# Kernel optimization log

Measured on AMD Instinct MI355X. Metric: run time of the kernel, lower is better.

The kernel has to match this reference:

```python
import jax, jax.numpy as jnp
import numpy as np

B, N = 16, 4096
D_IN, D_OUT, HID, E = 128, 128, 256, 8
SG_HID = 16  # SharedGate hidden fixed at 16 in __init__


def setup_inputs() -> dict:
    key = jax.random.key(0)
    ks = jax.random.split(key, 6)
    s = 0.05
    return {
        "x": jax.random.normal(ks[0], (B, N, D_IN), dtype=jnp.float32),
        "active_experts": jnp.ones((B, E), dtype=jnp.int32),
        # SharedGate: fc1 [16, D_IN], fc2 [D_IN, 16] (torch Linear weight is [out, in])
        "sg_w1": jax.random.normal(ks[1], (SG_HID, D_IN), dtype=jnp.float32) * s,
        "sg_w2": jax.random.normal(ks[2], (D_IN, SG_HID), dtype=jnp.float32) * s,
        # TaskSpecificGate: E linears [1, D_IN] -> stacked [E, D_IN]
        "gate_w": jax.random.normal(ks[3], (E, D_IN), dtype=jnp.float32) * s,
        # Expert MLPs (no bias): fc1 [E, HID, D_IN], fc2 [E, D_OUT, HID]
        "exp_w1": jax.random.normal(ks[4], (E, HID, D_IN), dtype=jnp.float32) * s,
        "exp_w2": jax.random.normal(ks[5], (E, D_OUT, HID), dtype=jnp.float32) * s,
    }


def reference(x, active_experts, sg_w1, sg_w2, gate_w, exp_w1, exp_w2):
    b, n, d_in = x.shape
    xf = x.reshape(-1, d_in)  # [T, D_IN], T = B*N (node-level routing)

    # SharedGate with residual: fc2(relu(fc1(x))) + x
    shared = jnp.maximum(xf @ sg_w1.T, 0.0) @ sg_w2.T + xf  # [T, D_IN]

    # Task-specific gate: per-expert scalar scores, masked softmax over experts
    scores = (shared @ gate_w.T).reshape(b, n, -1)  # [B, N, E]
    mask = active_experts.astype(bool)[:, None, :]  # [B, 1, E]
    masked = jnp.where(mask, scores, -jnp.inf)
    weights = jax.nn.softmax(masked, axis=-1)  # [B, N, E]

    # All experts (dense): batched two-layer MLP per expert
    h = jnp.maximum(jnp.einsum("td,ehd->teh", xf, exp_w1), 0.0)  # [T, E, HID]
    out = jnp.einsum("teh,eoh->teo", h, exp_w2)  # [T, E, D_OUT]
    out_r = out.reshape(b, n, weights.shape[-1], -1)  # [B, N, E, D_OUT]

    # Gate-weighted combine over experts
    output_end = jnp.sum(out_r * weights[..., None], axis=2)  # [B, N, D_OUT]
    aux_loss = jnp.float32(0.0)  # sign=False
    return output_end, aux_loss
```

## Files before the change

kernel.cpp:

```cpp
#include <hip/hip_runtime.h>
#include <hip/hip_bf16.h>


typedef float f32x4 __attribute__((ext_vector_type(4)));
typedef short bf16x8 __attribute__((ext_vector_type(8)));

static __device__ __forceinline__ short f2bs(float f) {
  union { __hip_bfloat16 b; short s; } u;
  u.b = __float2bfloat16(f);
  return u.s;
}

static __device__ __forceinline__ unsigned pk2(float lo, float hi) {
  union { __hip_bfloat162 b; unsigned u; } t;
  t.b = __float22bfloat162_rn(make_float2(lo, hi));
  return t.u;
}


__global__ void prep_kernel(const float* __restrict__ sg_w1,
                            const float* __restrict__ sg_w2,
                            const float* __restrict__ gate_w,
                            const float* __restrict__ exp_w1,
                            const float* __restrict__ exp_w2,
                            short* __restrict__ ws_s) {
  int idx = blockIdx.x * 256 + threadIdx.x;
  if (idx < 262144) {
    int e = idx >> 15, rem = idx & 32767;
    int frag = rem >> 9, lane = (rem >> 3) & 63, j = rem & 7;
    int hid = (frag >> 2) * 16 + (lane & 15);
    int k   = (frag & 3) * 32 + (lane >> 4) * 8 + j;
    ws_s[idx] = f2bs(exp_w1[(e * 256 + hid) * 128 + k]);
  } else if (idx < 524288) {
    int i2 = idx - 262144;
    int e = i2 >> 15, rem = i2 & 32767;
    int frag = rem >> 9, lane = (rem >> 3) & 63, j = rem & 7;
    int lg = lane >> 4, l15 = lane & 15;
    int ks = frag >> 3;
    int oi = frag & 7;
    int o  = oi * 16 + l15;
    int h  = ks * 32 + (j < 4 ? lg * 4 + j : 16 + lg * 4 + (j - 4));
    ws_s[idx] = f2bs(exp_w2[(e * 128 + o) * 256 + h]);
  } else if (idx < 526336) {
    int i3 = idx - 524288;
    int k = i3 >> 9, lane = (i3 >> 3) & 63, j = i3 & 7;
    int lg = lane >> 4, l15 = lane & 15;
    ws_s[idx] = f2bs(sg_w1[l15 * 128 + k * 32 + lg * 8 + j]);
  } else if (idx < 528384) {
    int i4 = idx - 526336;
    int k = i4 >> 9, lane = (i4 >> 3) & 63, j = i4 & 7;
    int lg = lane >> 4, l15 = lane & 15;
    ws_s[idx] = (l15 < 8) ? f2bs(gate_w[l15 * 128 + k * 32 + lg * 8 + j]) : (short)0;
  } else if (idx < 528896) {
    int i5 = idx - 528384;
    int lane = (i5 >> 3) & 63, j = i5 & 7;
    int lg = lane >> 4, l15 = lane & 15;
    int kk = lg * 8 + j;
    if (l15 < 8 && kk < 16) {
      float acc = 0.f;
      for (int d = 0; d < 128; ++d) acc += gate_w[l15 * 128 + d] * sg_w2[d * 16 + kk];
      ws_s[idx] = f2bs(acc);
    } else {
      ws_s[idx] = 0;
    }
  }
}

__global__ __launch_bounds__(256, 2) void moe_kernel(
    const float* __restrict__ x, const int* __restrict__ active,
    const short* __restrict__ ws_s, float* __restrict__ out) {
  __shared__ __align__(16) short Abuf[2][4096];
  __shared__ short Ul[4][1280];

  const short* W1p  = ws_s;
  const short* W2p  = ws_s + 262144;
  const short* sg1p = ws_s + 524288;
  const short* gwp  = ws_s + 526336;
  const short* gcp  = ws_s + 528384;

  const int tid  = threadIdx.x;
  const int lane = tid & 63;
  const int wid  = tid >> 6;
  const int l15  = lane & 15;
  const int lg   = lane >> 4;
  const int tokw = blockIdx.x * 128 + wid * 32;

  auto stageA = [&](int buf, int c) {
#pragma unroll
    for (int t = 0; t < 2; ++t) {
      int i = wid * 2 + t;
      const short* s = W1p + ((size_t)c * 8 + i) * 512 + lane * 8;
      __builtin_amdgcn_global_load_lds(
          (const __attribute__((address_space(1))) void*)s,
          (__attribute__((address_space(3))) void*)(&Abuf[buf][i * 512]),
          16, 0, 0);
    }
  };
  auto loadB = [&](bf16x8 (&B)[8], int c) {
    const short* p = W2p + (size_t)c * 4096 + lane * 8;
#pragma unroll
    for (int oi = 0; oi < 8; ++oi)
      B[oi] = *(const bf16x8*)(p + oi * 512);
  };

  stageA(0, 0);

  short* Ulw = &Ul[wid][0];
  for (int i = lane; i < 640; i += 64) ((int*)Ulw)[i] = 0;

  bf16x8 xf[2][4];
  {
    int trow = tokw + l15;
#pragma unroll
    for (int m = 0; m < 2; ++m) {
      const float* xr = x + (size_t)(trow + m * 16) * 128;
#pragma unroll
      for (int k = 0; k < 4; ++k) {
        int c = k * 32 + lg * 8;
        float4 a = *(const float4*)(xr + c);
        float4 b = *(const float4*)(xr + c + 4);
        bf16x8 v;
        v[0] = f2bs(a.x); v[1] = f2bs(a.y); v[2] = f2bs(a.z); v[3] = f2bs(a.w);
        v[4] = f2bs(b.x); v[5] = f2bs(b.y); v[6] = f2bs(b.z); v[7] = f2bs(b.w);
        xf[m][k] = v;
      }
    }
  }
  __syncthreads();

  f32x4 wreg[2];
  {
    bf16x8 sgf[4], gwf[4];
#pragma unroll
    for (int k = 0; k < 4; ++k) {
      sgf[k] = *(const bf16x8*)(sg1p + k * 512 + lane * 8);
      gwf[k] = *(const bf16x8*)(gwp  + k * 512 + lane * 8);
    }
#pragma unroll
    for (int m = 0; m < 2; ++m) {
      f32x4 acc = {0.f, 0.f, 0.f, 0.f};
#pragma unroll
      for (int k = 0; k < 4; ++k)
        acc = __builtin_amdgcn_mfma_f32_16x16x32_bf16(xf[m][k], sgf[k], acc, 0, 0, 0);
#pragma unroll
      for (int r = 0; r < 4; ++r)
        Ulw[(m * 16 + lg * 4 + r) * 40 + l15] = f2bs(fmaxf(acc[r], 0.f));
    }
    f32x4 sc[2];
#pragma unroll
    for (int m = 0; m < 2; ++m) {
      f32x4 acc = {0.f, 0.f, 0.f, 0.f};
#pragma unroll
      for (int k = 0; k < 4; ++k)
        acc = __builtin_amdgcn_mfma_f32_16x16x32_bf16(xf[m][k], gwf[k], acc, 0, 0, 0);
      sc[m] = acc;
    }
    __syncthreads();
    bf16x8 gcf = *(const bf16x8*)(gcp + lane * 8);
#pragma unroll
    for (int m = 0; m < 2; ++m) {
      bf16x8 uf = *(const bf16x8*)(Ulw + (m * 16 + l15) * 40 + lg * 8);
      sc[m] = __builtin_amdgcn_mfma_f32_16x16x32_bf16(uf, gcf, sc[m], 0, 0, 0);
    }
    int b = tokw >> 12;
    float am = (l15 < 8 && active[b * 8 + l15] != 0) ? 0.f : -3.0e38f;
#pragma unroll
    for (int m = 0; m < 2; ++m) {
      f32x4 w4;
#pragma unroll
      for (int r = 0; r < 4; ++r) {
        float s = sc[m][r] + am;
        float mx = s;
        mx = fmaxf(mx, __shfl_xor(mx, 1));
        mx = fmaxf(mx, __shfl_xor(mx, 2));
        mx = fmaxf(mx, __shfl_xor(mx, 4));
        float p = __expf(s - mx);
        float su = p;
        su += __shfl_xor(su, 1);
        su += __shfl_xor(su, 2);
        su += __shfl_xor(su, 4);
        w4[r] = p / su;
      }
      wreg[m] = w4;
    }
  }

  f32x4 acc2[2][8];
#pragma unroll
  for (int m = 0; m < 2; ++m)
#pragma unroll
    for (int o = 0; o < 8; ++o)
      acc2[m][o] = {0.f, 0.f, 0.f, 0.f};

  bf16x8 Ba[8], Bb[8];
  loadB(Ba, 0);

  for (int e = 0; e < 8; ++e) {
    float wv[2];
    {
      int srcb = ((l15 >> 2) << 4) | e;
      int rp = l15 & 3;
#pragma unroll
      for (int m = 0; m < 2; ++m) {
        float q0 = __shfl(wreg[m][0], srcb), q1 = __shfl(wreg[m][1], srcb);
        float q2 = __shfl(wreg[m][2], srcb), q3 = __shfl(wreg[m][3], srcb);
        float lo = (rp & 1) ? q1 : q0, hi = (rp & 1) ? q3 : q2;
        wv[m] = (rp & 2) ? hi : lo;
      }
    }

    auto chunk_body = [&](bf16x8 (&Bcur)[8], bf16x8 (&Bnext)[8], int bufA, int c) {
      if (c < 63) {
        stageA(bufA ^ 1, c + 1);
        loadB(Bnext, c + 1);
      }
      bf16x8 Af[8];
#pragma unroll
      for (int i = 0; i < 8; ++i)
        Af[i] = *(const bf16x8*)(&Abuf[bufA][i * 512 + lane * 8]);

      f32x4 a1[2][2];
#pragma unroll
      for (int m = 0; m < 2; ++m)
#pragma unroll
        for (int n = 0; n < 2; ++n) {
          f32x4 acc = {0.f, 0.f, 0.f, 0.f};
#pragma unroll
          for (int kx = 0; kx < 4; ++kx)
            acc = __builtin_amdgcn_mfma_f32_16x16x32_bf16(Af[n * 4 + kx], xf[m][kx], acc, 0, 0, 0);
          a1[m][n] = acc;
        }
      bf16x8 hB[2];
#pragma unroll
      for (int m = 0; m < 2; ++m) {
        float s = wv[m];
        union { unsigned u[4]; bf16x8 v; } hb;
        hb.u[0] = pk2(fmaxf(a1[m][0][0], 0.f) * s, fmaxf(a1[m][0][1], 0.f) * s);
        hb.u[1] = pk2(fmaxf(a1[m][0][2], 0.f) * s, fmaxf(a1[m][0][3], 0.f) * s);
        hb.u[2] = pk2(fmaxf(a1[m][1][0], 0.f) * s, fmaxf(a1[m][1][1], 0.f) * s);
        hb.u[3] = pk2(fmaxf(a1[m][1][2], 0.f) * s, fmaxf(a1[m][1][3], 0.f) * s);
        hB[m] = hb.v;
      }
#pragma unroll
      for (int o = 0; o < 8; ++o)
#pragma unroll
        for (int m = 0; m < 2; ++m)
          acc2[m][o] = __builtin_amdgcn_mfma_f32_16x16x32_bf16(Bcur[o], hB[m], acc2[m][o], 0, 0, 0);

      __syncthreads();
    };

#pragma unroll
    for (int kk = 0; kk < 4; ++kk) {
      int c0 = e * 8 + 2 * kk;
      chunk_body(Ba, Bb, 0, c0);
      chunk_body(Bb, Ba, 1, c0 + 1);
    }
  }

#pragma unroll
  for (int m = 0; m < 2; ++m)
#pragma unroll
    for (int o = 0; o < 8; ++o)
      *(f32x4*)(out + (size_t)(tokw + m * 16 + l15) * 128 + o * 16 + lg * 4) = acc2[m][o];

  if (blockIdx.x == 0 && tid == 0) out[8388608] = 0.0f;
}

extern "C" void kernel_launch(void* const* d_in, const int* in_sizes, int n_in,
                              void* d_out, int out_size, void* d_ws, size_t ws_size,
                              hipStream_t stream) {
  const float* x      = (const float*)d_in[0];
  const int*   act    = (const int*)d_in[1];
  const float* sg_w1  = (const float*)d_in[2];
  const float* sg_w2  = (const float*)d_in[3];
  const float* gate_w = (const float*)d_in[4];
  const float* exp_w1 = (const float*)d_in[5];
  const float* exp_w2 = (const float*)d_in[6];
  short* ws_s = (short*)d_ws;
  float* out = (float*)d_out;

  prep_kernel<<<2066, 256, 0, stream>>>(sg_w1, sg_w2, gate_w, exp_w1, exp_w2, ws_s);
  moe_kernel<<<512, 256, 0, stream>>>(x, act, ws_s, out);
}
```

Before: 92.59 us.

## Stage W1 and W2 chunks through a 4-deep LDS ring with prefetch distance 2

Replaces the double-buffered W1 LDS staging plus per-wave W2 register loads with a 4-slot LDS ring that holds both W1 and W2 chunks. Each chunk is fetched two iterations ahead with global_load_lds, and explicit vmcnt waits plus one barrier per chunk replace the trailing __syncthreads. The goal is deeper overlap of weight fetch with MFMA work and four times fewer redundant per-wave global reads of W2. The cost is LDS growing from 16KB to 64KB per block, which could limit the two-blocks-per-CU occupancy, and the hand-counted vmcnt values must match the number of outstanding loads.

Result: faster. 82.47 us (-10.9%).

```diff
diff --git a/kernel.cpp b/kernel.cpp
--- a/kernel.cpp
+++ b/kernel.cpp
@@ -69,7 +69,7 @@
 __global__ __launch_bounds__(256, 2) void moe_kernel(
     const float* __restrict__ x, const int* __restrict__ active,
     const short* __restrict__ ws_s, float* __restrict__ out) {
-  __shared__ __align__(16) short Abuf[2][4096];
+  __shared__ __align__(16) short Wring[4][8192];
   __shared__ short Ul[4][1280];
 
   const short* W1p  = ws_s;
@@ -85,25 +85,29 @@
   const int lg   = lane >> 4;
   const int tokw = blockIdx.x * 128 + wid * 32;
 
-  auto stageA = [&](int buf, int c) {
-#pragma unroll
-    for (int t = 0; t < 2; ++t) {
-      int i = wid * 2 + t;
-      const short* s = W1p + ((size_t)c * 8 + i) * 512 + lane * 8;
+  auto stage = [&](int c) {
+    int buf = c & 3;
+#pragma unroll
+    for (int t = 0; t < 4; ++t) {
+      int f = wid * 4 + t;
+      const short* s = (f < 8)
+          ? (W1p + ((size_t)c * 8 + f) * 512 + lane * 8)
+          : (W2p + ((size_t)c * 8 + (f - 8)) * 512 + lane * 8);
       __builtin_amdgcn_global_load_lds(
           (const __attribute__((address_space(1))) void*)s,
-          (__attribute__((address_space(3))) void*)(&Abuf[buf][i * 512]),
+          (__attribute__((address_space(3))) void*)(&Wring[buf][f * 512]),
           16, 0, 0);
     }
   };
-  auto loadB = [&](bf16x8 (&B)[8], int c) {
-    const short* p = W2p + (size_t)c * 4096 + lane * 8;
-#pragma unroll
-    for (int oi = 0; oi < 8; ++oi)
-      B[oi] = *(const bf16x8*)(p + oi * 512);
+  auto waitv = [&](int n) {
+    if (n == 8)      asm volatile("s_waitcnt vmcnt(8)" ::: "memory");
+    else if (n == 4) asm volatile("s_waitcnt vmcnt(4)" ::: "memory");
+    else             asm volatile("s_waitcnt vmcnt(0)" ::: "memory");
+    __builtin_amdgcn_sched_barrier(0);
   };
 
-  stageA(0, 0);
+  stage(0);
+  stage(1);
 
   short* Ulw = &Ul[wid][0];
   for (int i = lane; i < 640; i += 64) ((int*)Ulw)[i] = 0;
@@ -192,9 +196,6 @@
     for (int o = 0; o < 8; ++o)
       acc2[m][o] = {0.f, 0.f, 0.f, 0.f};
 
-  bf16x8 Ba[8], Bb[8];
-  loadB(Ba, 0);
-
   for (int e = 0; e < 8; ++e) {
     float wv[2];
     {
@@ -209,15 +210,20 @@
       }
     }
 
-    auto chunk_body = [&](bf16x8 (&Bcur)[8], bf16x8 (&Bnext)[8], int bufA, int c) {
-      if (c < 63) {
-        stageA(bufA ^ 1, c + 1);
-        loadB(Bnext, c + 1);
-      }
-      bf16x8 Af[8];
-#pragma unroll
-      for (int i = 0; i < 8; ++i)
-        Af[i] = *(const bf16x8*)(&Abuf[bufA][i * 512 + lane * 8]);
+#pragma unroll
+    for (int ks = 0; ks < 8; ++ks) {
+      const int c = e * 8 + ks;
+      if (c + 2 < 64) stage(c + 2);
+      waitv(c <= 61 ? 8 : (c == 62 ? 4 : 0));
+      __builtin_amdgcn_s_barrier();
+
+      const short* wb = &Wring[c & 3][0];
+      bf16x8 Af[8], Bf[8];
+#pragma unroll
+      for (int i = 0; i < 8; ++i) {
+        Af[i] = *(const bf16x8*)(wb + i * 512 + lane * 8);
+        Bf[i] = *(const bf16x8*)(wb + 4096 + i * 512 + lane * 8);
+      }
 
       f32x4 a1[2][2];
 #pragma unroll
@@ -245,16 +251,7 @@
       for (int o = 0; o < 8; ++o)
 #pragma unroll
         for (int m = 0; m < 2; ++m)
-          acc2[m][o] = __builtin_amdgcn_mfma_f32_16x16x32_bf16(Bcur[o], hB[m], acc2[m][o], 0, 0, 0);
-
-      __syncthreads();
-    };
-
-#pragma unroll
-    for (int kk = 0; kk < 4; ++kk) {
-      int c0 = e * 8 + 2 * kk;
-      chunk_body(Ba, Bb, 0, c0);
-      chunk_body(Bb, Ba, 1, c0 + 1);
+          acc2[m][o] = __builtin_amdgcn_mfma_f32_16x16x32_bf16(Bf[o], hB[m], acc2[m][o], 0, 0, 0);
     }
   }
 
```
